# Kernel optimization log

Measured on AMD Instinct MI355X. Metric: run time of the kernel, lower is better.

## Reference

```python
import jax, jax.numpy as jnp
import numpy as np

W_MAE, W_GRAD, W_TV, W_BG, W_MSE = 1.0, 0.1, 0.002, 0.15, 1.0
EPS = 1e-8


def setup_inputs() -> dict:
    key = jax.random.key(0)
    k1, k2, k3 = jax.random.split(key, 3)
    B, C, D, H, W = 2, 3, 128, 128, 128
    pred = jax.random.normal(k1, (B, C, D, H, W), dtype=jnp.float32)
    target = jax.random.normal(k2, (B, C, D, H, W), dtype=jnp.float32)
    # binary foreground mask, broadcast over channels
    mask = (jax.random.uniform(k3, (B, 1, D, H, W)) > 0.5).astype(jnp.float32)
    return {"pred": pred, "target": target, "mask": mask}


def _grad3(x):
    dx = x[:, :, 1:, :, :] - x[:, :, :-1, :, :]
    dy = x[:, :, :, 1:, :] - x[:, :, :, :-1, :]
    dz = x[:, :, :, :, 1:] - x[:, :, :, :, :-1]
    return dx, dy, dz


def reference(pred, target, mask):
    C = pred.shape[1]

    def masked_mean(x, m):
        return (x * m).sum() / (m.sum() * C + EPS)

    pred_in = pred * mask
    tgt_in = target * mask
    diff = pred_in - tgt_in

    l_mae = masked_mean(jnp.abs(diff), mask)

    px, py, pz = _grad3(pred_in)
    tx, ty, tz = _grad3(tgt_in)
    mx = jnp.minimum(mask[:, :, 1:, :, :], mask[:, :, :-1, :, :])
    my = jnp.minimum(mask[:, :, :, 1:, :], mask[:, :, :, :-1, :])
    mz = jnp.minimum(mask[:, :, :, :, 1:], mask[:, :, :, :, :-1])

    l_grad = (masked_mean(jnp.abs(px - tx), mx)
              + masked_mean(jnp.abs(py - ty), my)
              + masked_mean(jnp.abs(pz - tz), mz))
    l_tv = (masked_mean(jnp.abs(px), mx)
            + masked_mean(jnp.abs(py), my)
            + masked_mean(jnp.abs(pz), mz))

    inv = 1.0 - mask
    l_bg = (jnp.abs(pred) * inv).sum() / (inv.sum() * C + EPS)

    l_mse = masked_mean(diff ** 2, mask)

    return (W_MAE * l_mae + W_GRAD * l_grad + W_TV * l_tv
            + W_BG * l_bg + W_MSE * l_mse)
```

## Files before the change

kernel.cpp:

```cpp
#include <hip/hip_runtime.h>

#define NACC 13
#define NPAD 16
#define NBLOCKS 12288
#define NMID 48

__device__ __forceinline__ float4 ld4(const float* p) {
    return *reinterpret_cast<const float4*>(p);
}

__global__ __launch_bounds__(256) void loss_main(
    const float* __restrict__ pred, const float* __restrict__ target,
    const float* __restrict__ mask, float* __restrict__ partials)
{
    float acc[NACC];
#pragma unroll
    for (int k = 0; k < NACC; ++k) acc[k] = 0.f;

    const float4 z4 = make_float4(0.f, 0.f, 0.f, 0.f);

    const int g  = blockIdx.x * 256 + threadIdx.x;
    const int w4 = g & 31;
    const int h  = (g >> 5) & 127;
    const int d  = (g >> 12) & 127;
    const int bc = g >> 19;
    const int b  = bc & 1;
    const int c  = bc >> 1;
    const int w  = w4 << 2;
    const int sp = d * 16384 + h * 128 + w;
    const int mb = b * 2097152 + sp;
    const int pb = (b * 3 + c) * 2097152 + sp;
    const bool hw = w4 < 31, hh = h < 127, hd = d < 127;

    const float4 m0  = ld4(mask + mb);
    const float4 mh  = hh ? ld4(mask + mb + 128)   : z4;
    const float4 md  = hd ? ld4(mask + mb + 16384) : z4;
    const float4 p0  = ld4(pred + pb);
    const float4 t0  = ld4(target + pb);
    const float4 ph  = hh ? ld4(pred + pb + 128)     : z4;
    const float4 th  = hh ? ld4(target + pb + 128)   : z4;
    const float4 pd  = hd ? ld4(pred + pb + 16384)   : z4;
    const float4 td  = hd ? ld4(target + pb + 16384) : z4;
    float m4w = 0.f, p4 = 0.f, t4 = 0.f;
    if (hw) { m4w = mask[mb + 4]; p4 = pred[pb + 4]; t4 = target[pb + 4]; }

    const float mz0 = fminf(m0.x, m0.y), mz1 = fminf(m0.y, m0.z),
                mz2 = fminf(m0.z, m0.w), mz3 = fminf(m0.w, m4w);
    const float my0 = fminf(m0.x, mh.x), my1 = fminf(m0.y, mh.y),
                my2 = fminf(m0.z, mh.z), my3 = fminf(m0.w, mh.w);
    const float mx0 = fminf(m0.x, md.x), mx1 = fminf(m0.y, md.y),
                mx2 = fminf(m0.z, md.z), mx3 = fminf(m0.w, md.w);

    acc[0] = m0.x + m0.y + m0.z + m0.w;
    acc[1] = mx0 + mx1 + mx2 + mx3;
    acc[2] = my0 + my1 + my2 + my3;
    acc[3] = mz0 + mz1 + mz2 + mz3;

    const float e0x = p0.x - t0.x, e0y = p0.y - t0.y,
                e0z = p0.z - t0.z, e0w = p0.w - t0.w;
    const float e4  = p4 - t4;

    acc[4] = fabsf(e0x)*m0.x + fabsf(e0y)*m0.y
           + fabsf(e0z)*m0.z + fabsf(e0w)*m0.w;
    acc[5] = e0x*e0x*m0.x + e0y*e0y*m0.y
           + e0z*e0z*m0.z + e0w*e0w*m0.w;
    acc[6] = fabsf(p0.x)*(1.f-m0.x) + fabsf(p0.y)*(1.f-m0.y)
           + fabsf(p0.z)*(1.f-m0.z) + fabsf(p0.w)*(1.f-m0.w);

    acc[9]  = fabsf(e0y-e0x)*mz0 + fabsf(e0z-e0y)*mz1
            + fabsf(e0w-e0z)*mz2 + fabsf(e4 -e0w)*mz3;
    acc[12] = fabsf(p0.y-p0.x)*mz0 + fabsf(p0.z-p0.y)*mz1
            + fabsf(p0.w-p0.z)*mz2 + fabsf(p4  -p0.w)*mz3;

    acc[8]  = fabsf((ph.x-th.x)-e0x)*my0 + fabsf((ph.y-th.y)-e0y)*my1
            + fabsf((ph.z-th.z)-e0z)*my2 + fabsf((ph.w-th.w)-e0w)*my3;
    acc[11] = fabsf(ph.x-p0.x)*my0 + fabsf(ph.y-p0.y)*my1
            + fabsf(ph.z-p0.z)*my2 + fabsf(ph.w-p0.w)*my3;

    acc[7]  = fabsf((pd.x-td.x)-e0x)*mx0 + fabsf((pd.y-td.y)-e0y)*mx1
            + fabsf((pd.z-td.z)-e0z)*mx2 + fabsf((pd.w-td.w)-e0w)*mx3;
    acc[10] = fabsf(pd.x-p0.x)*mx0 + fabsf(pd.y-p0.y)*mx1
            + fabsf(pd.z-p0.z)*mx2 + fabsf(pd.w-p0.w)*mx3;

    const int lane = threadIdx.x & 63;
    const int wave = threadIdx.x >> 6;
    __shared__ float red[4][NACC];
#pragma unroll
    for (int k = 0; k < NACC; ++k) {
        float v = acc[k];
        for (int o = 32; o > 0; o >>= 1) v += __shfl_down(v, o, 64);
        if (lane == 0) red[wave][k] = v;
    }
    __syncthreads();
    if (threadIdx.x < NPAD) {
        const int k = threadIdx.x;
        const float v = (k < NACC)
            ? red[0][k] + red[1][k] + red[2][k] + red[3][k] : 0.f;
        partials[blockIdx.x * NPAD + k] = v;
    }
}

__global__ __launch_bounds__(256) void loss_mid(
    const float* __restrict__ partials, float* __restrict__ mid)
{
    const int r = blockIdx.x * 256 + threadIdx.x;
    const float* row = partials + r * NPAD;
    const float4 r0 = ld4(row);     const float4 r1 = ld4(row + 4);
    const float4 r2 = ld4(row + 8); const float4 r3 = ld4(row + 12);
    float acc[NPAD] = {r0.x, r0.y, r0.z, r0.w, r1.x, r1.y, r1.z, r1.w,
                       r2.x, r2.y, r2.z, r2.w, r3.x, r3.y, r3.z, r3.w};

    const int lane = threadIdx.x & 63;
    const int wave = threadIdx.x >> 6;
    __shared__ float red[4][NPAD];
#pragma unroll
    for (int k = 0; k < NPAD; ++k) {
        float v = acc[k];
        for (int o = 32; o > 0; o >>= 1) v += __shfl_down(v, o, 64);
        if (lane == 0) red[wave][k] = v;
    }
    __syncthreads();
    if (threadIdx.x < NPAD) {
        const int k = threadIdx.x;
        mid[blockIdx.x * NPAD + k] =
            red[0][k] + red[1][k] + red[2][k] + red[3][k];
    }
}

__global__ __launch_bounds__(64) void loss_final(
    const float* __restrict__ mid, float* __restrict__ out)
{
    const int lane = threadIdx.x;
    float acc[NPAD];
#pragma unroll
    for (int k = 0; k < NPAD; ++k) acc[k] = 0.f;
    if (lane < NMID) {
        const float* row = mid + lane * NPAD;
        const float4 r0 = ld4(row);     const float4 r1 = ld4(row + 4);
        const float4 r2 = ld4(row + 8); const float4 r3 = ld4(row + 12);
        acc[0] = r0.x;  acc[1] = r0.y;  acc[2] = r0.z;  acc[3] = r0.w;
        acc[4] = r1.x;  acc[5] = r1.y;  acc[6] = r1.z;  acc[7] = r1.w;
        acc[8] = r2.x;  acc[9] = r2.y;  acc[10] = r2.z; acc[11] = r2.w;
        acc[12] = r3.x; acc[13] = r3.y; acc[14] = r3.z; acc[15] = r3.w;
    }
#pragma unroll
    for (int k = 0; k < NACC; ++k) {
        for (int o = 32; o > 0; o >>= 1) acc[k] += __shfl_down(acc[k], o, 64);
    }
    if (lane == 0) {
        const float EPS = 1e-8f;
        float loss = (acc[4] + acc[5]) / (acc[0] + EPS);
        loss += 0.1f   * (acc[7] / (acc[1] + EPS) + acc[8] / (acc[2] + EPS)
                        + acc[9] / (acc[3] + EPS));
        loss += 0.002f * (acc[10] / (acc[1] + EPS) + acc[11] / (acc[2] + EPS)
                        + acc[12] / (acc[3] + EPS));
        const float inv3 = 12582912.f - acc[0];
        loss += 0.15f * acc[6] / (inv3 + EPS);
        out[0] = loss;
    }
}

extern "C" void kernel_launch(void* const* d_in, const int* in_sizes, int n_in,
                              void* d_out, int out_size, void* d_ws, size_t ws_size,
                              hipStream_t stream) {
    const float* pred   = (const float*)d_in[0];
    const float* target = (const float*)d_in[1];
    const float* mask   = (const float*)d_in[2];
    float* out      = (float*)d_out;
    float* partials = (float*)d_ws;
    float* mid      = partials + NBLOCKS * NPAD;

    loss_main<<<NBLOCKS, 256, 0, stream>>>(pred, target, mask, partials);
    loss_mid<<<NMID, 256, 0, stream>>>(partials, mid);
    loss_final<<<1, 64, 0, stream>>>(mid, out);
}
```

Before: 157.7 us.

## Loop over channels per thread to reuse mask loads across channels

Each thread now handles all three channels for one spatial location, loading the mask and its neighbours once and reusing the derived min-masks. Grid and block sizes shrink accordingly, and the final normalisation multiplies mask sums by three. This cuts redundant mask traffic and halves the number of per-block reductions per element, at the cost of fewer threads in flight and more registers per thread.

```diff
diff --git a/kernel.cpp b/kernel.cpp
--- a/kernel.cpp
+++ b/kernel.cpp
@@ -2,14 +2,14 @@
 
 #define NACC 13
 #define NPAD 16
-#define NBLOCKS 12288
-#define NMID 48
+#define NBLOCKS 8192
+#define NMID 32
 
 __device__ __forceinline__ float4 ld4(const float* p) {
     return *reinterpret_cast<const float4*>(p);
 }
 
-__global__ __launch_bounds__(256) void loss_main(
+__global__ __launch_bounds__(128) void loss_main(
     const float* __restrict__ pred, const float* __restrict__ target,
     const float* __restrict__ mask, float* __restrict__ partials)
 {
@@ -19,30 +19,20 @@
 
     const float4 z4 = make_float4(0.f, 0.f, 0.f, 0.f);
 
-    const int g  = blockIdx.x * 256 + threadIdx.x;
+    const int g  = blockIdx.x * 128 + threadIdx.x;
     const int w4 = g & 31;
     const int h  = (g >> 5) & 127;
     const int d  = (g >> 12) & 127;
-    const int bc = g >> 19;
-    const int b  = bc & 1;
-    const int c  = bc >> 1;
+    const int b  = g >> 19;
     const int w  = w4 << 2;
-    const int sp = d * 16384 + h * 128 + w;
-    const int mb = b * 2097152 + sp;
-    const int pb = (b * 3 + c) * 2097152 + sp;
+    const int mb  = b * 2097152 + d * 16384 + h * 128 + w;
+    const int pb0 = b * 6291456 + d * 16384 + h * 128 + w;
     const bool hw = w4 < 31, hh = h < 127, hd = d < 127;
 
     const float4 m0  = ld4(mask + mb);
+    const float  m4w = hw ? mask[mb + 4] : 0.f;
     const float4 mh  = hh ? ld4(mask + mb + 128)   : z4;
     const float4 md  = hd ? ld4(mask + mb + 16384) : z4;
-    const float4 p0  = ld4(pred + pb);
-    const float4 t0  = ld4(target + pb);
-    const float4 ph  = hh ? ld4(pred + pb + 128)     : z4;
-    const float4 th  = hh ? ld4(target + pb + 128)   : z4;
-    const float4 pd  = hd ? ld4(pred + pb + 16384)   : z4;
-    const float4 td  = hd ? ld4(target + pb + 16384) : z4;
-    float m4w = 0.f, p4 = 0.f, t4 = 0.f;
-    if (hw) { m4w = mask[mb + 4]; p4 = pred[pb + 4]; t4 = target[pb + 4]; }
 
     const float mz0 = fminf(m0.x, m0.y), mz1 = fminf(m0.y, m0.z),
                 mz2 = fminf(m0.z, m0.w), mz3 = fminf(m0.w, m4w);
@@ -56,35 +46,48 @@
     acc[2] = my0 + my1 + my2 + my3;
     acc[3] = mz0 + mz1 + mz2 + mz3;
 
-    const float e0x = p0.x - t0.x, e0y = p0.y - t0.y,
-                e0z = p0.z - t0.z, e0w = p0.w - t0.w;
-    const float e4  = p4 - t4;
+#pragma unroll
+    for (int c = 0; c < 3; ++c) {
+        const int pb = pb0 + c * 2097152;
+        const float4 p0 = ld4(pred + pb);
+        const float4 t0 = ld4(target + pb);
+        float p4 = 0.f, t4 = 0.f;
+        if (hw) { p4 = pred[pb + 4]; t4 = target[pb + 4]; }
+        const float4 ph = hh ? ld4(pred + pb + 128)     : z4;
+        const float4 th = hh ? ld4(target + pb + 128)   : z4;
+        const float4 pd = hd ? ld4(pred + pb + 16384)   : z4;
+        const float4 td = hd ? ld4(target + pb + 16384) : z4;
 
-    acc[4] = fabsf(e0x)*m0.x + fabsf(e0y)*m0.y
-           + fabsf(e0z)*m0.z + fabsf(e0w)*m0.w;
-    acc[5] = e0x*e0x*m0.x + e0y*e0y*m0.y
-           + e0z*e0z*m0.z + e0w*e0w*m0.w;
-    acc[6] = fabsf(p0.x)*(1.f-m0.x) + fabsf(p0.y)*(1.f-m0.y)
-           + fabsf(p0.z)*(1.f-m0.z) + fabsf(p0.w)*(1.f-m0.w);
+        const float e0x = p0.x - t0.x, e0y = p0.y - t0.y,
+                    e0z = p0.z - t0.z, e0w = p0.w - t0.w;
+        const float e4  = p4 - t4;
 
-    acc[9]  = fabsf(e0y-e0x)*mz0 + fabsf(e0z-e0y)*mz1
-            + fabsf(e0w-e0z)*mz2 + fabsf(e4 -e0w)*mz3;
-    acc[12] = fabsf(p0.y-p0.x)*mz0 + fabsf(p0.z-p0.y)*mz1
-            + fabsf(p0.w-p0.z)*mz2 + fabsf(p4  -p0.w)*mz3;
+        acc[4] += fabsf(e0x)*m0.x + fabsf(e0y)*m0.y
+                + fabsf(e0z)*m0.z + fabsf(e0w)*m0.w;
+        acc[5] += e0x*e0x*m0.x + e0y*e0y*m0.y
+                + e0z*e0z*m0.z + e0w*e0w*m0.w;
+        acc[6] += fabsf(p0.x)*(1.f-m0.x) + fabsf(p0.y)*(1.f-m0.y)
+                + fabsf(p0.z)*(1.f-m0.z) + fabsf(p0.w)*(1.f-m0.w);
 
-    acc[8]  = fabsf((ph.x-th.x)-e0x)*my0 + fabsf((ph.y-th.y)-e0y)*my1
-            + fabsf((ph.z-th.z)-e0z)*my2 + fabsf((ph.w-th.w)-e0w)*my3;
-    acc[11] = fabsf(ph.x-p0.x)*my0 + fabsf(ph.y-p0.y)*my1
-            + fabsf(ph.z-p0.z)*my2 + fabsf(ph.w-p0.w)*my3;
+        acc[9]  += fabsf(e0y-e0x)*mz0 + fabsf(e0z-e0y)*mz1
+                 + fabsf(e0w-e0z)*mz2 + fabsf(e4 -e0w)*mz3;
+        acc[12] += fabsf(p0.y-p0.x)*mz0 + fabsf(p0.z-p0.y)*mz1
+                 + fabsf(p0.w-p0.z)*mz2 + fabsf(p4  -p0.w)*mz3;
 
-    acc[7]  = fabsf((pd.x-td.x)-e0x)*mx0 + fabsf((pd.y-td.y)-e0y)*mx1
-            + fabsf((pd.z-td.z)-e0z)*mx2 + fabsf((pd.w-td.w)-e0w)*mx3;
-    acc[10] = fabsf(pd.x-p0.x)*mx0 + fabsf(pd.y-p0.y)*mx1
-            + fabsf(pd.z-p0.z)*mx2 + fabsf(pd.w-p0.w)*mx3;
+        acc[8]  += fabsf((ph.x-th.x)-e0x)*my0 + fabsf((ph.y-th.y)-e0y)*my1
+                 + fabsf((ph.z-th.z)-e0z)*my2 + fabsf((ph.w-th.w)-e0w)*my3;
+        acc[11] += fabsf(ph.x-p0.x)*my0 + fabsf(ph.y-p0.y)*my1
+                 + fabsf(ph.z-p0.z)*my2 + fabsf(ph.w-p0.w)*my3;
+
+        acc[7]  += fabsf((pd.x-td.x)-e0x)*mx0 + fabsf((pd.y-td.y)-e0y)*mx1
+                 + fabsf((pd.z-td.z)-e0z)*mx2 + fabsf((pd.w-td.w)-e0w)*mx3;
+        acc[10] += fabsf(pd.x-p0.x)*mx0 + fabsf(pd.y-p0.y)*mx1
+                 + fabsf(pd.z-p0.z)*mx2 + fabsf(pd.w-p0.w)*mx3;
+    }
 
     const int lane = threadIdx.x & 63;
     const int wave = threadIdx.x >> 6;
-    __shared__ float red[4][NACC];
+    __shared__ float red[2][NACC];
 #pragma unroll
     for (int k = 0; k < NACC; ++k) {
         float v = acc[k];
@@ -94,8 +97,7 @@
     __syncthreads();
     if (threadIdx.x < NPAD) {
         const int k = threadIdx.x;
-        const float v = (k < NACC)
-            ? red[0][k] + red[1][k] + red[2][k] + red[3][k] : 0.f;
+        const float v = (k < NACC) ? red[0][k] + red[1][k] : 0.f;
         partials[blockIdx.x * NPAD + k] = v;
     }
 }
@@ -149,13 +151,14 @@
     }
     if (lane == 0) {
         const float EPS = 1e-8f;
-        float loss = (acc[4] + acc[5]) / (acc[0] + EPS);
-        loss += 0.1f   * (acc[7] / (acc[1] + EPS) + acc[8] / (acc[2] + EPS)
-                        + acc[9] / (acc[3] + EPS));
-        loss += 0.002f * (acc[10] / (acc[1] + EPS) + acc[11] / (acc[2] + EPS)
-                        + acc[12] / (acc[3] + EPS));
-        const float inv3 = 12582912.f - acc[0];
-        loss += 0.15f * acc[6] / (inv3 + EPS);
+        const float M = acc[0], Mx = acc[1], My = acc[2], Mz = acc[3];
+        float loss = (acc[4] + acc[5]) / (3.f * M + EPS);
+        loss += 0.1f   * (acc[7] / (3.f*Mx + EPS) + acc[8] / (3.f*My + EPS)
+                        + acc[9] / (3.f*Mz + EPS));
+        loss += 0.002f * (acc[10] / (3.f*Mx + EPS) + acc[11] / (3.f*My + EPS)
+                        + acc[12] / (3.f*Mz + EPS));
+        const float inv = 4194304.f - M;
+        loss += 0.15f * acc[6] / (3.f * inv + EPS);
         out[0] = loss;
     }
 }
@@ -170,7 +173,7 @@
     float* partials = (float*)d_ws;
     float* mid      = partials + NBLOCKS * NPAD;
 
-    loss_main<<<NBLOCKS, 256, 0, stream>>>(pred, target, mask, partials);
+    loss_main<<<NBLOCKS, 128, 0, stream>>>(pred, target, mask, partials);
     loss_mid<<<NMID, 256, 0, stream>>>(partials, mid);
     loss_final<<<1, 64, 0, stream>>>(mid, out);
 }
```

Measured after the change: 145.4 us. -7.8%, faster.
